# Optimization experiments

Hardware: AMD Instinct MI355X
Metric: run time of the kernel (lower is better)

Reference implementation:

```python
import jax, jax.numpy as jnp
import numpy as np

L = 3          # num_legs
D = 32         # leg_dim == out_leg_dim (output_dim = input_dim = D**L)
NUM_NODES = 6  # num_levels * (num_legs - 1) = 3 * 2
B = 256        # batch


def setup_inputs() -> dict:
    key = jax.random.key(0)
    k1, k2 = jax.random.split(key, 2)
    inputs = jax.random.normal(k1, (B, D ** L), dtype=jnp.float32)
    # all 6 entangler nodes share shape (D,D,D,D) since leg_dim == out_leg_dim;
    # scale ~ 1/D to mimic glorot and keep the 6-contraction chain numerically sane
    nodes = jax.random.normal(k2, (NUM_NODES, D, D, D, D), dtype=jnp.float32) / D
    bias = jnp.zeros((D ** L,), dtype=jnp.float32)
    return {"inputs": inputs, "nodes": nodes, "bias": bias}


def reference(inputs, nodes, bias):
    # Faithful port of DenseEntangler.call: reshape the input vector to L legs,
    # then contract NUM_NODES 4-leg tensors; node i eats edge slots (i%L, (i+1)%L)
    # with its axes (0,1) and replaces them with its axes (2,3).
    # jnp.tensordot output axis order (free axes of x in order, then node axes 2,3)
    # matches tn.contract_between's default ordering, so the final flatten is identical.
    Bn = inputs.shape[0]
    x = inputs.reshape((Bn,) + (D,) * L)   # axis 0 = batch, axes 1..L = legs
    pos = list(range(1, L + 1))            # edge slot k -> current axis of x
    for i in range(NUM_NODES):
        s0, s1 = i % L, (i + 1) % L
        p, q = pos[s0], pos[s1]
        x = jnp.tensordot(x, nodes[i], axes=[[p, q], [0, 1]])
        # remaining axes of x keep order (batch stays axis 0); new node axes go last
        new_pos = [0] * L
        for k in range(L):
            if k == s0:
                new_pos[k] = L - 1
            elif k == s1:
                new_pos[k] = L
            else:
                a = pos[k]
                new_pos[k] = a - (p < a) - (q < a)
        pos = new_pos
    out = x.reshape(Bn, -1) + bias  # flatten in current axis order, as in the TF code
    return jax.nn.relu(out)
```

## Files before the change

kernel.cpp:

```cpp
#include <hip/hip_runtime.h>
#include <hip/hip_bf16.h>
#include <stdint.h>

using bf16 = __hip_bfloat16;
typedef __attribute__((ext_vector_type(8))) short short8;
typedef __attribute__((ext_vector_type(4))) float floatx4;

#define DD 32
#define DL3 32768
#define BATCH 256
#define NK 1024

__device__ __forceinline__ void load16(const void* g, void* l) {
  __builtin_amdgcn_global_load_lds((const __attribute__((address_space(1))) void*)g,
                                   (__attribute__((address_space(3))) void*)l,
                                   16, 0, 0);
}

__global__ void prep_x(const float* __restrict__ x, bf16* __restrict__ dst) {
  int b = blockIdx.x >> 5, v = blockIdx.x & 31;
  __shared__ float tile[32][33];
  const float* xb = x + (size_t)b * DL3 + v * DD;
  int t = threadIdx.x;
#pragma unroll
  for (int it = 0; it < 4; ++it) {
    int u = (t >> 5) + it * 8, f = t & 31;
    tile[u][f] = xb[u * NK + f];
  }
  __syncthreads();
  bf16* db = dst + (size_t)b * DL3 + v * NK;
#pragma unroll
  for (int it = 0; it < 4; ++it) {
    int f = (t >> 5) + it * 8, u = t & 31;
    db[f * DD + u] = __float2bfloat16(tile[u][f]);
  }
}

__global__ void prep_nodes(const float* __restrict__ nodes, bf16* __restrict__ dst) {
  int id = blockIdx.x;
  int nb = id & 31, kb = (id >> 5) & 31, i = id >> 10;
  const float* src = nodes + (size_t)i * 1048576;
  bf16* d = dst + (size_t)i * 1048576;
  __shared__ float tile[32][33];
  int t = threadIdx.x;
#pragma unroll
  for (int it = 0; it < 4; ++it) {
    int u = (t >> 5) + it * 8, j = t & 31;
    tile[u][j] = src[(size_t)(u * 32 + kb) * 1024 + nb * 32 + j];
  }
  __syncthreads();
#pragma unroll
  for (int it = 0; it < 4; ++it) {
    int j = (t >> 5) + it * 8, u = t & 31;
    d[(size_t)(nb * 32 + j) * 1024 + kb * 32 + u] = __float2bfloat16(tile[u][j]);
  }
}

template <bool FINAL>
__global__ __launch_bounds__(256) void entangler_gemm(
    const bf16* __restrict__ A, const bf16* __restrict__ Bn,
    bf16* __restrict__ Cb, float* __restrict__ Cf, const float* __restrict__ bias) {
  __shared__ bf16 sA[128 * 32];
  __shared__ bf16 sB[128 * 32];
  const int t = threadIdx.x;
  const int lane = t & 63;
  const int lane16 = lane & 15, quad = lane >> 4;
  const int w = t >> 6;
  const int m0 = (w >> 1) * 64, n0 = (w & 1) * 64;
  const int b0 = blockIdx.x * 4;
  const int N0 = blockIdx.y * 128;

  floatx4 acc[4][4];
#pragma unroll
  for (int i = 0; i < 4; ++i)
#pragma unroll
    for (int j = 0; j < 4; ++j)
      acc[i][j] = (floatx4){0.f, 0.f, 0.f, 0.f};

  const bf16* Ab = A + (size_t)b0 * DL3;
  const bf16* Bb = Bn + (size_t)N0 * NK;

  for (int kv = 0; kv < 32; ++kv) {
    __syncthreads();
#pragma unroll
    for (int r = 0; r < 2; ++r) {
      int idx = r * 256 + t;
      load16(Ab + (size_t)(idx >> 7) * DL3 + kv * NK + (idx & 127) * 8, sA + idx * 8);
      load16(Bb + (size_t)(idx >> 2) * NK + kv * 32 + (idx & 3) * 8, sB + idx * 8);
    }
    __syncthreads();

    short8 af[4], bfr[4];
#pragma unroll
    for (int i = 0; i < 4; ++i)
      af[i] = *(const short8*)(sA + (m0 + i * 16 + lane16) * 32 + quad * 8);
#pragma unroll
    for (int j = 0; j < 4; ++j)
      bfr[j] = *(const short8*)(sB + (n0 + j * 16 + lane16) * 32 + quad * 8);
#pragma unroll
    for (int i = 0; i < 4; ++i)
#pragma unroll
      for (int j = 0; j < 4; ++j)
        acc[i][j] = __builtin_amdgcn_mfma_f32_16x16x32_bf16(af[i], bfr[j], acc[i][j], 0, 0, 0);
  }

  const int R0 = blockIdx.x * 128;
#pragma unroll
  for (int i = 0; i < 4; ++i) {
#pragma unroll
    for (int j = 0; j < 4; ++j) {
#pragma unroll
      for (int r = 0; r < 4; ++r) {
        int row = R0 + m0 + i * 16 + quad * 4 + r;
        int col = N0 + n0 + j * 16 + lane16;
        if (FINAL) {
          float v = acc[i][j][r] + bias[(row & 31) * 1024 + col];
          Cf[(size_t)row * 1024 + col] = fmaxf(v, 0.f);
        } else {
          Cb[(size_t)row * 1024 + col] = __float2bfloat16(acc[i][j][r]);
        }
      }
    }
  }
}

extern "C" void kernel_launch(void* const* d_in, const int* in_sizes, int n_in,
                              void* d_out, int out_size, void* d_ws, size_t ws_size,
                              hipStream_t stream) {
  const float* x     = (const float*)d_in[0];
  const float* nodes = (const float*)d_in[1];
  const float* bias  = (const float*)d_in[2];
  float* out = (float*)d_out;

  bf16* buf0  = (bf16*)d_ws;
  bf16* buf1  = buf0 + (size_t)BATCH * DL3;
  bf16* nodeT = buf1 + (size_t)BATCH * DL3;

  prep_x<<<dim3(BATCH * 32), dim3(256), 0, stream>>>(x, buf0);
  prep_nodes<<<dim3(6 * 1024), dim3(256), 0, stream>>>(nodes, nodeT);

  dim3 grid(64, 8), blk(256);
  entangler_gemm<false><<<grid, blk, 0, stream>>>(buf0, nodeT + (size_t)0 * 1048576, buf1, nullptr, nullptr);
  entangler_gemm<false><<<grid, blk, 0, stream>>>(buf1, nodeT + (size_t)1 * 1048576, buf0, nullptr, nullptr);
  entangler_gemm<false><<<grid, blk, 0, stream>>>(buf0, nodeT + (size_t)2 * 1048576, buf1, nullptr, nullptr);
  entangler_gemm<false><<<grid, blk, 0, stream>>>(buf1, nodeT + (size_t)3 * 1048576, buf0, nullptr, nullptr);
  entangler_gemm<false><<<grid, blk, 0, stream>>>(buf0, nodeT + (size_t)4 * 1048576, buf1, nullptr, nullptr);
  entangler_gemm<true ><<<grid, blk, 0, stream>>>(buf1, nodeT + (size_t)5 * 1048576, nullptr, out, bias);
}
```

Baseline: 257.7 us.

## Drop LDS staging and prefetch MFMA fragments directly from global into registers

```diff
diff --git a/kernel.cpp b/kernel.cpp
--- a/kernel.cpp
+++ b/kernel.cpp
@@ -11,13 +11,7 @@
 #define BATCH 256
 #define NK 1024
 
-__device__ __forceinline__ void load16(const void* g, void* l) {
-  __builtin_amdgcn_global_load_lds((const __attribute__((address_space(1))) void*)g,
-                                   (__attribute__((address_space(3))) void*)l,
-                                   16, 0, 0);
-}
-
-__global__ void prep_x(const float* __restrict__ x, bf16* __restrict__ dst) {
+__global__ __launch_bounds__(256) void prep_x(const float* __restrict__ x, bf16* __restrict__ dst) {
   int b = blockIdx.x >> 5, v = blockIdx.x & 31;
   __shared__ float tile[32][33];
   const float* xb = x + (size_t)b * DL3 + v * DD;
@@ -36,7 +30,7 @@
   }
 }
 
-__global__ void prep_nodes(const float* __restrict__ nodes, bf16* __restrict__ dst) {
+__global__ __launch_bounds__(256) void prep_nodes(const float* __restrict__ nodes, bf16* __restrict__ dst) {
   int id = blockIdx.x;
   int nb = id & 31, kb = (id >> 5) & 31, i = id >> 10;
   const float* src = nodes + (size_t)i * 1048576;
@@ -57,18 +51,25 @@
 }
 
 template <bool FINAL>
-__global__ __launch_bounds__(256) void entangler_gemm(
+__global__ __launch_bounds__(256, 2) void entangler_gemm(
     const bf16* __restrict__ A, const bf16* __restrict__ Bn,
     bf16* __restrict__ Cb, float* __restrict__ Cf, const float* __restrict__ bias) {
-  __shared__ bf16 sA[128 * 32];
-  __shared__ bf16 sB[128 * 32];
   const int t = threadIdx.x;
   const int lane = t & 63;
   const int lane16 = lane & 15, quad = lane >> 4;
   const int w = t >> 6;
-  const int m0 = (w >> 1) * 64, n0 = (w & 1) * 64;
-  const int b0 = blockIdx.x * 4;
-  const int N0 = blockIdx.y * 128;
+  const int n0 = w * 64;
+  const int b0 = blockIdx.x * 2;
+  const int N0 = blockIdx.y * 256;
+
+  const bf16* aBase[4];
+#pragma unroll
+  for (int i = 0; i < 4; ++i)
+    aBase[i] = A + (size_t)(b0 + (i >> 1)) * DL3 + ((i & 1) * 16 + lane16) * 32 + quad * 8;
+  const bf16* bBase[4];
+#pragma unroll
+  for (int j = 0; j < 4; ++j)
+    bBase[j] = Bn + (size_t)(N0 + n0 + j * 16 + lane16) * NK + quad * 8;
 
   floatx4 acc[4][4];
 #pragma unroll
@@ -77,41 +78,42 @@
     for (int j = 0; j < 4; ++j)
       acc[i][j] = (floatx4){0.f, 0.f, 0.f, 0.f};
 
-  const bf16* Ab = A + (size_t)b0 * DL3;
-  const bf16* Bb = Bn + (size_t)N0 * NK;
+  short8 af[3][4], bfr[3][4];
 
+#pragma unroll
+  for (int s = 0; s < 2; ++s)
+#pragma unroll
+    for (int i = 0; i < 4; ++i) {
+      af[s][i]  = *(const short8*)(aBase[i] + s * NK);
+      bfr[s][i] = *(const short8*)(bBase[i] + s * 32);
+    }
+
+#pragma unroll
   for (int kv = 0; kv < 32; ++kv) {
-    __syncthreads();
+    if (kv + 2 < 32) {
+      const int sl = (kv + 2) % 3;
 #pragma unroll
-    for (int r = 0; r < 2; ++r) {
-      int idx = r * 256 + t;
-      load16(Ab + (size_t)(idx >> 7) * DL3 + kv * NK + (idx & 127) * 8, sA + idx * 8);
-      load16(Bb + (size_t)(idx >> 2) * NK + kv * 32 + (idx & 3) * 8, sB + idx * 8);
+      for (int i = 0; i < 4; ++i) {
+        af[sl][i]  = *(const short8*)(aBase[i] + (kv + 2) * NK);
+        bfr[sl][i] = *(const short8*)(bBase[i] + (kv + 2) * 32);
+      }
     }
-    __syncthreads();
-
-    short8 af[4], bfr[4];
-#pragma unroll
-    for (int i = 0; i < 4; ++i)
-      af[i] = *(const short8*)(sA + (m0 + i * 16 + lane16) * 32 + quad * 8);
-#pragma unroll
-    for (int j = 0; j < 4; ++j)
-      bfr[j] = *(const short8*)(sB + (n0 + j * 16 + lane16) * 32 + quad * 8);
+    const int s = kv % 3;
 #pragma unroll
     for (int i = 0; i < 4; ++i)
 #pragma unroll
       for (int j = 0; j < 4; ++j)
-        acc[i][j] = __builtin_amdgcn_mfma_f32_16x16x32_bf16(af[i], bfr[j], acc[i][j], 0, 0, 0);
+        acc[i][j] = __builtin_amdgcn_mfma_f32_16x16x32_bf16(af[s][i], bfr[s][j], acc[i][j], 0, 0, 0);
   }
 
-  const int R0 = blockIdx.x * 128;
+  const int R0 = blockIdx.x * 64;
 #pragma unroll
   for (int i = 0; i < 4; ++i) {
 #pragma unroll
     for (int j = 0; j < 4; ++j) {
 #pragma unroll
       for (int r = 0; r < 4; ++r) {
-        int row = R0 + m0 + i * 16 + quad * 4 + r;
+        int row = R0 + i * 16 + quad * 4 + r;
         int col = N0 + n0 + j * 16 + lane16;
         if (FINAL) {
           float v = acc[i][j][r] + bias[(row & 31) * 1024 + col];
@@ -139,7 +141,7 @@
   prep_x<<<dim3(BATCH * 32), dim3(256), 0, stream>>>(x, buf0);
   prep_nodes<<<dim3(6 * 1024), dim3(256), 0, stream>>>(nodes, nodeT);
 
-  dim3 grid(64, 8), blk(256);
+  dim3 grid(128, 4), blk(256);
   entangler_gemm<false><<<grid, blk, 0, stream>>>(buf0, nodeT + (size_t)0 * 1048576, buf1, nullptr, nullptr);
   entangler_gemm<false><<<grid, blk, 0, stream>>>(buf1, nodeT + (size_t)1 * 1048576, buf0, nullptr, nullptr);
   entangler_gemm<false><<<grid, blk, 0, stream>>>(buf0, nodeT + (size_t)2 * 1048576, buf1, nullptr, nullptr);
```

After: 429.7 us. 1.67x slower.
